# Optimization experiments

Hardware: AMD Instinct MI355X
Metric: run time of the kernel (lower is better)

## Reference

```python
import jax, jax.numpy as jnp
import numpy as np

B, L, V, D = 4096, 128, 50257, 64
NEG_INF = -1e9
COS_EPS = 1e-8  # torch cosine_similarity default eps


def setup_inputs() -> dict:
    key = jax.random.key(0)
    k1, k2, k3, k4, k5, k6 = jax.random.split(key, 6)
    return {
        "ids_a": jax.random.randint(k1, (B, L), 0, V, dtype=jnp.int64) if jax.config.jax_enable_x64 else jax.random.randint(k1, (B, L), 0, V, dtype=jnp.int32),
        "mask_a": jax.random.randint(k2, (B, L), 0, 2, dtype=jnp.int32),
        "ids_b": jax.random.randint(k3, (B, L), 0, V, dtype=jnp.int32),
        "mask_b": jax.random.randint(k4, (B, L), 0, 2, dtype=jnp.int32),
        "mu_table": jax.random.normal(k5, (V, D), dtype=jnp.float32),
        "feat_table": jax.random.normal(k6, (V, D), dtype=jnp.float32),
    }


def _side(ids, mask, mu_table, feat_table):
    # Embedding gathers: [B, L, D]
    mu = mu_table[ids]
    feat = feat_table[ids]
    m = mask.astype(mu.dtype)  # [B, L]
    # render_mean_pool: masked mean of mu -> query [B, D]
    denom = jnp.maximum(m.sum(axis=1, keepdims=True), 1.0)
    q = jnp.einsum('bld,bl->bd', mu, m) / denom
    # render_softmax_attention: single-query masked softmax over mu keys
    scores = jnp.einsum('bld,bd->bl', mu, q)
    scores = jnp.where(mask.astype(bool), scores, NEG_INF)
    attn = jax.nn.softmax(scores, axis=-1)  # [B, L]
    return jnp.einsum('bl,bld->bd', attn, feat)  # weighted sum of feat


def reference(ids_a, mask_a, ids_b, mask_b, mu_table, feat_table):
    mean_a = _side(ids_a, mask_a, mu_table, feat_table)
    mean_b = _side(ids_b, mask_b, mu_table, feat_table)
    # torch cosine_similarity: x.y / (max(||x||, eps) * max(||y||, eps))
    na = jnp.maximum(jnp.linalg.norm(mean_a, axis=-1), COS_EPS)
    nb = jnp.maximum(jnp.linalg.norm(mean_b, axis=-1), COS_EPS)
    cos = jnp.sum(mean_a * mean_b, axis=-1) / (na * nb)
    return cos * 5.0
```

## Files before the change

kernel.cpp:

```cpp
#include <hip/hip_runtime.h>
#include <hip/hip_fp16.h>
#include <math.h>

#define BB 4096
#define LL 128
#define DD 64
#define VV 50257
#define TAB_ELEMS (VV * DD)

__global__ __launch_bounds__(256) void convert_tables_kernel(
    const float* __restrict__ mu, const float* __restrict__ feat,
    __half* __restrict__ out_mu, __half* __restrict__ out_feat)
{
    const int n4 = TAB_ELEMS / 4;
    for (int i = blockIdx.x * blockDim.x + threadIdx.x; i < n4;
         i += gridDim.x * blockDim.x) {
        const float4 m = ((const float4*)mu)[i];
        const float4 f = ((const float4*)feat)[i];
        union { __half2 h[2]; uint2 u; } pm, pf;
        pm.h[0] = __floats2half2_rn(m.x, m.y);
        pm.h[1] = __floats2half2_rn(m.z, m.w);
        pf.h[0] = __floats2half2_rn(f.x, f.y);
        pf.h[1] = __floats2half2_rn(f.z, f.w);
        ((uint2*)out_mu)[i]   = pm.u;
        ((uint2*)out_feat)[i] = pf.u;
    }
}

__device__ __forceinline__ float4 load_row4(const __half* __restrict__ tab,
                                            int id, int c4) {
    const uint2 raw = ((const uint2*)(tab + (size_t)id * DD))[c4];
    const float2 f01 = __half22float2(*(const __half2*)&raw.x);
    const float2 f23 = __half22float2(*(const __half2*)&raw.y);
    return make_float4(f01.x, f01.y, f23.x, f23.y);
}

__global__ __launch_bounds__(256, 8) void softmax_attn_cos_kernel(
    const int* __restrict__ ids_a, const int* __restrict__ mask_a,
    const int* __restrict__ ids_b, const int* __restrict__ mask_b,
    const __half* __restrict__ mu_table, const __half* __restrict__ feat_table,
    float* __restrict__ out)
{
    __shared__ int    s_ids[2][LL];
    __shared__ float  s_msk[2][LL];
    __shared__ float4 s_q[2][16];
    __shared__ float4 s_qp[2][2][16];
    __shared__ float  s_sc[2][LL];
    __shared__ float4 s_op[2][2][16];
    __shared__ float  s_mean[2][DD];
    __shared__ float  s_sum[2];
    __shared__ int    s_nm[2];

    const int tid  = threadIdx.x;
    const int lane = tid & 63;
    const int wave = tid >> 6;
    const int side = wave >> 1;
    const int wsub = wave & 1;
    const int grp  = lane >> 4;
    const int c4   = lane & 15;
    const int b    = blockIdx.x;

    {
        const int si = tid >> 7;
        const int l  = tid & 127;
        const int* idp = si ? ids_b  : ids_a;
        const int* mp  = si ? mask_b : mask_a;
        s_ids[si][l] = idp[b * LL + l];
        s_msk[si][l] = (float)mp[b * LL + l];
    }
    __syncthreads();

    {
        float4 qp = make_float4(0.f, 0.f, 0.f, 0.f);
        #pragma unroll
        for (int it = 0; it < 16; ++it) {
            const int r = wsub * 64 + it * 4 + grp;
            if (s_msk[side][r] > 0.5f) {
                const float4 f = load_row4(mu_table, s_ids[side][r], c4);
                qp.x += f.x; qp.y += f.y; qp.z += f.z; qp.w += f.w;
            }
        }
        #pragma unroll
        for (int off = 16; off <= 32; off <<= 1) {
            qp.x += __shfl_xor(qp.x, off, 64);
            qp.y += __shfl_xor(qp.y, off, 64);
            qp.z += __shfl_xor(qp.z, off, 64);
            qp.w += __shfl_xor(qp.w, off, 64);
        }
        if (lane < 16) s_qp[side][wsub][c4] = qp;
    }
    __syncthreads();

    if (tid < 128) {
        const int si = tid >> 6;
        const int dd = tid & 63;
        float mv = s_msk[si][dd] + s_msk[si][dd + 64];
        #pragma unroll
        for (int off = 32; off; off >>= 1) mv += __shfl_xor(mv, off, 64);
        if (dd == 0) s_nm[si] = (int)(mv + 0.5f);
        const float denom = fmaxf(mv, 1.0f);
        if (dd < 16) {
            float4 q0 = s_qp[si][0][dd], q1 = s_qp[si][1][dd];
            float4 q;
            q.x = (q0.x + q1.x) / denom; q.y = (q0.y + q1.y) / denom;
            q.z = (q0.z + q1.z) / denom; q.w = (q0.w + q1.w) / denom;
            s_q[si][dd] = q;
        }
    }
    __syncthreads();

    {
        const float4 q4 = s_q[side][c4];
        #pragma unroll
        for (int it = 0; it < 16; ++it) {
            const int r = wsub * 64 + it * 4 + grp;
            float sc = -1e9f;
            if (s_msk[side][r] > 0.5f) {
                const float4 f = load_row4(mu_table, s_ids[side][r], c4);
                sc = f.x * q4.x + f.y * q4.y + f.z * q4.z + f.w * q4.w;
                #pragma unroll
                for (int off = 1; off <= 8; off <<= 1)
                    sc += __shfl_xor(sc, off, 64);
            }
            if (c4 == 0) s_sc[side][r] = sc;
        }
    }
    __syncthreads();

    if (wsub == 0) {
        const float s1 = s_sc[side][lane], s2 = s_sc[side][lane + 64];
        float mx = fmaxf(s1, s2);
        #pragma unroll
        for (int off = 32; off; off >>= 1) mx = fmaxf(mx, __shfl_xor(mx, off, 64));
        const float e1 = expf(s1 - mx), e2 = expf(s2 - mx);
        s_sc[side][lane] = e1; s_sc[side][lane + 64] = e2;
        float sm = e1 + e2;
        #pragma unroll
        for (int off = 32; off; off >>= 1) sm += __shfl_xor(sm, off, 64);
        if (lane == 0) s_sum[side] = sm;
    }
    __syncthreads();

    {
        const bool allm = (s_nm[side] == 0);
        float4 op = make_float4(0.f, 0.f, 0.f, 0.f);
        #pragma unroll
        for (int it = 0; it < 16; ++it) {
            const int r = wsub * 64 + it * 4 + grp;
            if (allm || s_msk[side][r] > 0.5f) {
                const float w  = s_sc[side][r];
                const float4 f = load_row4(feat_table, s_ids[side][r], c4);
                op.x = fmaf(f.x, w, op.x); op.y = fmaf(f.y, w, op.y);
                op.z = fmaf(f.z, w, op.z); op.w = fmaf(f.w, w, op.w);
            }
        }
        #pragma unroll
        for (int off = 16; off <= 32; off <<= 1) {
            op.x += __shfl_xor(op.x, off, 64);
            op.y += __shfl_xor(op.y, off, 64);
            op.z += __shfl_xor(op.z, off, 64);
            op.w += __shfl_xor(op.w, off, 64);
        }
        if (lane < 16) s_op[side][wsub][c4] = op;
    }
    __syncthreads();

    if (tid < 32) {
        const int si = tid >> 4, cc = tid & 15;
        const float inv = 1.0f / s_sum[si];
        float4 o0 = s_op[si][0][cc], o1 = s_op[si][1][cc];
        float4 o;
        o.x = (o0.x + o1.x) * inv; o.y = (o0.y + o1.y) * inv;
        o.z = (o0.z + o1.z) * inv; o.w = (o0.w + o1.w) * inv;
        ((float4*)&s_mean[si][0])[cc] = o;
    }
    __syncthreads();

    if (tid < 64) {
        const float a = s_mean[0][tid], c = s_mean[1][tid];
        float dt = a * c, na = a * a, nb = c * c;
        #pragma unroll
        for (int off = 32; off; off >>= 1) {
            dt += __shfl_xor(dt, off, 64);
            na += __shfl_xor(na, off, 64);
            nb += __shfl_xor(nb, off, 64);
        }
        if (tid == 0) {
            const float denom = fmaxf(sqrtf(na), 1e-8f) * fmaxf(sqrtf(nb), 1e-8f);
            out[b] = 5.0f * dt / denom;
        }
    }
}

extern "C" void kernel_launch(void* const* d_in, const int* in_sizes, int n_in,
                              void* d_out, int out_size, void* d_ws, size_t ws_size,
                              hipStream_t stream) {
    const int*   ids_a  = (const int*)d_in[0];
    const int*   mask_a = (const int*)d_in[1];
    const int*   ids_b  = (const int*)d_in[2];
    const int*   mask_b = (const int*)d_in[3];
    const float* mu     = (const float*)d_in[4];
    const float* feat   = (const float*)d_in[5];
    float* out = (float*)d_out;

    __half* ws_mu   = (__half*)d_ws;
    __half* ws_feat = ws_mu + TAB_ELEMS;

    convert_tables_kernel<<<1024, 256, 0, stream>>>(mu, feat, ws_mu, ws_feat);
    softmax_attn_cos_kernel<<<BB, 256, 0, stream>>>(
        ids_a, mask_a, ids_b, mask_b, ws_mu, ws_feat, out);
}
```

Measured before the change: 136.8 us.

## Keep mu rows in registers, prefetch feat rows during scoring, use fdot2

Gathered mu rows are kept in registers from the query pass so the scoring pass no longer reloads them. Feat rows are loaded unconditionally during scoring, overlapping with the dot products, and then reused from registers in the weighted sum, which drops the mask branches. Scores use packed fp16 dot instructions with the query quantized to half. The extra registers lower the occupancy hint from 8 to 6, and feat is now gathered for masked rows too, adding memory traffic.

New measurement: 123.2 us. 1.11x faster.

```diff
diff --git a/kernel.cpp b/kernel.cpp
--- a/kernel.cpp
+++ b/kernel.cpp
@@ -7,6 +7,31 @@
 #define DD 64
 #define VV 50257
 #define TAB_ELEMS (VV * DD)
+
+typedef _Float16 h2_t __attribute__((ext_vector_type(2)));
+
+__device__ __forceinline__ float dot2acc(unsigned a, unsigned b, float c) {
+#if __has_builtin(__builtin_amdgcn_fdot2)
+    return __builtin_amdgcn_fdot2(__builtin_bit_cast(h2_t, a),
+                                  __builtin_bit_cast(h2_t, b), c, false);
+#else
+    const float2 fa = __half22float2(*(const __half2*)&a);
+    const float2 fb = __half22float2(*(const __half2*)&b);
+    return fmaf(fa.x, fb.x, fmaf(fa.y, fb.y, c));
+#endif
+}
+
+__device__ __forceinline__ float4 cvt_chunk(uint2 raw) {
+    const float2 f01 = __half22float2(*(const __half2*)&raw.x);
+    const float2 f23 = __half22float2(*(const __half2*)&raw.y);
+    return make_float4(f01.x, f01.y, f23.x, f23.y);
+}
+
+__device__ __forceinline__ unsigned pack_h2(float a, float b) {
+    union { __half2 h; unsigned u; } p;
+    p.h = __floats2half2_rn(a, b);
+    return p.u;
+}
 
 __global__ __launch_bounds__(256) void convert_tables_kernel(
     const float* __restrict__ mu, const float* __restrict__ feat,
@@ -17,39 +42,28 @@
          i += gridDim.x * blockDim.x) {
         const float4 m = ((const float4*)mu)[i];
         const float4 f = ((const float4*)feat)[i];
-        union { __half2 h[2]; uint2 u; } pm, pf;
-        pm.h[0] = __floats2half2_rn(m.x, m.y);
-        pm.h[1] = __floats2half2_rn(m.z, m.w);
-        pf.h[0] = __floats2half2_rn(f.x, f.y);
-        pf.h[1] = __floats2half2_rn(f.z, f.w);
-        ((uint2*)out_mu)[i]   = pm.u;
-        ((uint2*)out_feat)[i] = pf.u;
-    }
-}
-
-__device__ __forceinline__ float4 load_row4(const __half* __restrict__ tab,
-                                            int id, int c4) {
-    const uint2 raw = ((const uint2*)(tab + (size_t)id * DD))[c4];
-    const float2 f01 = __half22float2(*(const __half2*)&raw.x);
-    const float2 f23 = __half22float2(*(const __half2*)&raw.y);
-    return make_float4(f01.x, f01.y, f23.x, f23.y);
-}
-
-__global__ __launch_bounds__(256, 8) void softmax_attn_cos_kernel(
+        uint2 pm, pf;
+        pm.x = pack_h2(m.x, m.y); pm.y = pack_h2(m.z, m.w);
+        pf.x = pack_h2(f.x, f.y); pf.y = pack_h2(f.z, f.w);
+        ((uint2*)out_mu)[i]   = pm;
+        ((uint2*)out_feat)[i] = pf;
+    }
+}
+
+__global__ __launch_bounds__(256, 6) void softmax_attn_cos_kernel(
     const int* __restrict__ ids_a, const int* __restrict__ mask_a,
     const int* __restrict__ ids_b, const int* __restrict__ mask_b,
     const __half* __restrict__ mu_table, const __half* __restrict__ feat_table,
     float* __restrict__ out)
 {
-    __shared__ int    s_ids[2][LL];
-    __shared__ float  s_msk[2][LL];
-    __shared__ float4 s_q[2][16];
-    __shared__ float4 s_qp[2][2][16];
-    __shared__ float  s_sc[2][LL];
-    __shared__ float4 s_op[2][2][16];
-    __shared__ float  s_mean[2][DD];
-    __shared__ float  s_sum[2];
-    __shared__ int    s_nm[2];
+    __shared__ int      s_ids[2][LL];
+    __shared__ float    s_msk[2][LL];
+    __shared__ unsigned s_qh[2][32];
+    __shared__ float4   s_qp[2][2][16];
+    __shared__ float    s_sc[2][LL];
+    __shared__ float4   s_op[2][2][16];
+    __shared__ float    s_mean[2][DD];
+    __shared__ float    s_sum[2];
 
     const int tid  = threadIdx.x;
     const int lane = tid & 63;
@@ -70,14 +84,20 @@
     }
     __syncthreads();
 
+    uint2 v[16];
+    unsigned kept = 0;
     {
         float4 qp = make_float4(0.f, 0.f, 0.f, 0.f);
         #pragma unroll
         for (int it = 0; it < 16; ++it) {
             const int r = wsub * 64 + it * 4 + grp;
             if (s_msk[side][r] > 0.5f) {
-                const float4 f = load_row4(mu_table, s_ids[side][r], c4);
+                kept |= (1u << it);
+                v[it] = ((const uint2*)(mu_table + (size_t)s_ids[side][r] * DD))[c4];
+                const float4 f = cvt_chunk(v[it]);
                 qp.x += f.x; qp.y += f.y; qp.z += f.z; qp.w += f.w;
+            } else {
+                v[it] = make_uint2(0u, 0u);
             }
         }
         #pragma unroll
@@ -97,32 +117,31 @@
         float mv = s_msk[si][dd] + s_msk[si][dd + 64];
         #pragma unroll
         for (int off = 32; off; off >>= 1) mv += __shfl_xor(mv, off, 64);
-        if (dd == 0) s_nm[si] = (int)(mv + 0.5f);
         const float denom = fmaxf(mv, 1.0f);
         if (dd < 16) {
-            float4 q0 = s_qp[si][0][dd], q1 = s_qp[si][1][dd];
-            float4 q;
-            q.x = (q0.x + q1.x) / denom; q.y = (q0.y + q1.y) / denom;
-            q.z = (q0.z + q1.z) / denom; q.w = (q0.w + q1.w) / denom;
-            s_q[si][dd] = q;
-        }
-    }
-    __syncthreads();
-
-    {
-        const float4 q4 = s_q[side][c4];
+            const float4 q0 = s_qp[si][0][dd], q1 = s_qp[si][1][dd];
+            const float qx = (q0.x + q1.x) / denom, qy = (q0.y + q1.y) / denom;
+            const float qz = (q0.z + q1.z) / denom, qw = (q0.w + q1.w) / denom;
+            s_qh[si][2 * dd]     = pack_h2(qx, qy);
+            s_qh[si][2 * dd + 1] = pack_h2(qz, qw);
+        }
+    }
+    __syncthreads();
+
+    {
+        const uint2 qq = ((const uint2*)&s_qh[side][0])[c4];
         #pragma unroll
         for (int it = 0; it < 16; ++it) {
             const int r = wsub * 64 + it * 4 + grp;
-            float sc = -1e9f;
-            if (s_msk[side][r] > 0.5f) {
-                const float4 f = load_row4(mu_table, s_ids[side][r], c4);
-                sc = f.x * q4.x + f.y * q4.y + f.z * q4.z + f.w * q4.w;
-                #pragma unroll
-                for (int off = 1; off <= 8; off <<= 1)
-                    sc += __shfl_xor(sc, off, 64);
-            }
-            if (c4 == 0) s_sc[side][r] = sc;
+            float p = dot2acc(v[it].x, qq.x, 0.f);
+            p = dot2acc(v[it].y, qq.y, p);
+            const uint2 nf =
+                ((const uint2*)(feat_table + (size_t)s_ids[side][r] * DD))[c4];
+            #pragma unroll
+            for (int off = 1; off <= 8; off <<= 1)
+                p += __shfl_xor(p, off, 64);
+            if (c4 == 0) s_sc[side][r] = ((kept >> it) & 1u) ? p : -1e9f;
+            v[it] = nf;
         }
     }
     __syncthreads();
@@ -142,17 +161,14 @@
     __syncthreads();
 
     {
-        const bool allm = (s_nm[side] == 0);
         float4 op = make_float4(0.f, 0.f, 0.f, 0.f);
         #pragma unroll
         for (int it = 0; it < 16; ++it) {
             const int r = wsub * 64 + it * 4 + grp;
-            if (allm || s_msk[side][r] > 0.5f) {
-                const float w  = s_sc[side][r];
-                const float4 f = load_row4(feat_table, s_ids[side][r], c4);
-                op.x = fmaf(f.x, w, op.x); op.y = fmaf(f.y, w, op.y);
-                op.z = fmaf(f.z, w, op.z); op.w = fmaf(f.w, w, op.w);
-            }
+            const float w  = s_sc[side][r];
+            const float4 f = cvt_chunk(v[it]);
+            op.x = fmaf(f.x, w, op.x); op.y = fmaf(f.y, w, op.y);
+            op.z = fmaf(f.z, w, op.z); op.w = fmaf(f.w, w, op.w);
         }
         #pragma unroll
         for (int off = 16; off <= 32; off <<= 1) {
@@ -168,7 +184,7 @@
     if (tid < 32) {
         const int si = tid >> 4, cc = tid & 15;
         const float inv = 1.0f / s_sum[si];
-        float4 o0 = s_op[si][0][cc], o1 = s_op[si][1][cc];
+        const float4 o0 = s_op[si][0][cc], o1 = s_op[si][1][cc];
         float4 o;
         o.x = (o0.x + o1.x) * inv; o.y = (o0.y + o1.y) * inv;
         o.z = (o0.z + o1.z) * inv; o.w = (o0.w + o1.w) * inv;
```
